# Optimization experiments

Hardware: AMD Instinct MI355X
Metric: run time of the kernel (lower is better)

The kernel has to match this reference:

```python
import jax, jax.numpy as jnp
import numpy as np

B = 32768      # batch
S = 512        # state_dim
G = 128        # goal_dim
A = 32         # action_dim
P = 16         # num_primitives
H1, H2 = 512, 256        # big_model hidden sizes
VH1, VH2 = 1024, 512     # value hidden sizes


def _w(k, shape, scale=0.05):
    return jax.random.normal(k, shape, jnp.float32) * scale


def setup_inputs() -> dict:
    key = jax.random.key(0)
    ks = jax.random.split(key, 24)
    d = {"features": jax.random.normal(ks[0], (B, S + G), jnp.float32)}
    # state encoder: S->H1->H2
    d["se_w1"] = _w(ks[1], (S, H1));  d["se_b1"] = jnp.zeros((H1,), jnp.float32)
    d["se_w2"] = _w(ks[2], (H1, H2)); d["se_b2"] = jnp.zeros((H2,), jnp.float32)
    # goal encoder: G->H1->H2
    d["ge_w1"] = _w(ks[3], (G, H1));  d["ge_b1"] = jnp.zeros((H1,), jnp.float32)
    d["ge_w2"] = _w(ks[4], (H1, H2)); d["ge_b2"] = jnp.zeros((H2,), jnp.float32)
    # gate: 2*H2->H2->P (sigmoid)
    d["gt_w1"] = _w(ks[5], (2 * H2, H2)); d["gt_b1"] = jnp.zeros((H2,), jnp.float32)
    d["gt_w2"] = _w(ks[6], (H2, P));      d["gt_b2"] = jnp.zeros((P,), jnp.float32)
    # primitive state encoder: S->H1->H2
    d["pse_w1"] = _w(ks[7], (S, H1));  d["pse_b1"] = jnp.zeros((H1,), jnp.float32)
    d["pse_w2"] = _w(ks[8], (H1, H2)); d["pse_b2"] = jnp.zeros((H2,), jnp.float32)
    # P primitives, each H2->H2->2A (stacked for batched GEMM)
    d["pw1"] = _w(ks[9], (P, H2, H2));     d["pb1"] = jnp.zeros((P, H2), jnp.float32)
    d["pw2"] = _w(ks[10], (P, H2, 2 * A)); d["pb2"] = jnp.zeros((P, 2 * A), jnp.float32)
    # value net: (S+G)->VH1->VH2
    d["vf_w1"] = _w(ks[11], (S + G, VH1)); d["vf_b1"] = jnp.zeros((VH1,), jnp.float32)
    d["vf_w2"] = _w(ks[12], (VH1, VH2));   d["vf_b2"] = jnp.zeros((VH2,), jnp.float32)
    return d


def _mlp2(x, w1, b1, w2, b2):
    return jax.nn.relu(jax.nn.relu(x @ w1 + b1) @ w2 + b2)


def reference(features,
              se_w1, se_b1, se_w2, se_b2,
              ge_w1, ge_b1, ge_w2, ge_b2,
              gt_w1, gt_b1, gt_w2, gt_b2,
              pse_w1, pse_b1, pse_w2, pse_b2,
              pw1, pb1, pw2, pb2,
              vf_w1, vf_b1, vf_w2, vf_b2):
    state, goal = features[:, :S], features[:, S:]
    # gating weights
    s_emb = _mlp2(state, se_w1, se_b1, se_w2, se_b2)      # [B,H2]
    g_emb = _mlp2(goal, ge_w1, ge_b1, ge_w2, ge_b2)       # [B,H2]
    gate_in = jnp.concatenate([s_emb, g_emb], axis=-1)    # [B,2*H2]
    weights = jax.nn.sigmoid(jax.nn.relu(gate_in @ gt_w1 + gt_b1) @ gt_w2 + gt_b2)  # [B,P]
    # shared primitive embedding
    prim_embed = _mlp2(state, pse_w1, pse_b1, pse_w2, pse_b2)  # [B,H2]
    # all primitives as one batched GEMM
    h = jax.nn.relu(jnp.einsum('bh,phk->bpk', prim_embed, pw1) + pb1[None])  # [B,P,H2]
    out = jnp.einsum('bpk,pkd->bpd', h, pw2) + pb2[None]                      # [B,P,2A]
    mu, log_std = out[..., :A], out[..., A:]
    sigma = jnp.exp(log_std)
    # precision-weighted Gaussian mixture
    inv = weights[..., None] / sigma        # [B,P,A]
    denom = inv.sum(axis=1)                 # [B,A]
    mean = (inv * mu).sum(axis=1) / denom   # [B,A]  (learn_log_std=True -> mean only)
    # critic
    value = _mlp2(features, vf_w1, vf_b1, vf_w2, vf_b2)  # [B,VH2]
    return (mean, value)
```

## Files before the change

kernel.cpp:

```cpp
#include <hip/hip_runtime.h>
#include <stdint.h>

#define NB 32768

typedef __bf16 bf16x8 __attribute__((ext_vector_type(8)));
typedef float f32x4 __attribute__((ext_vector_type(4)));

__device__ __forceinline__ unsigned pack_bf2(float a, float b) {
  union { __bf16 h[2]; unsigned u; } t;
  t.h[0] = (__bf16)a; t.h[1] = (__bf16)b;
  return t.u;
}
__device__ __forceinline__ unsigned short bf16b(float f) {
  union { __bf16 h; unsigned short u; } t;
  t.h = (__bf16)f;
  return t.u;
}
__device__ __forceinline__ float bf2f(unsigned short h) {
  union { unsigned u; float f; } v; v.u = ((unsigned)h) << 16;
  return v.f;
}

__device__ __forceinline__ void gld_lds16(void* lds, const void* g) {
  __builtin_amdgcn_global_load_lds(
      (__attribute__((address_space(1))) unsigned int*)(uintptr_t)g,
      (__attribute__((address_space(3))) unsigned int*)(uintptr_t)lds,
      16, 0, 0);
}

__device__ __forceinline__ int xcd_swz(int bid, int nwg) {
  return (bid & 7) * (nwg >> 3) + (bid >> 3);
}


__global__ __launch_bounds__(256) void fconv_k(const float* __restrict__ src,
                                               unsigned short* __restrict__ dst) {
  size_t idx = ((size_t)blockIdx.x * 256 + threadIdx.x) * 8;
  float4 a = *(const float4*)(src + idx);
  float4 b = *(const float4*)(src + idx + 4);
  uint4 o;
  o.x = pack_bf2(a.x, a.y); o.y = pack_bf2(a.z, a.w);
  o.z = pack_bf2(b.x, b.y); o.w = pack_bf2(b.z, b.w);
  *(uint4*)(dst + idx) = o;
}

__global__ __launch_bounds__(256) void bcat_k(const float* __restrict__ a,
                                              const float* __restrict__ b,
                                              float* __restrict__ dst) {
  const int i = blockIdx.x * 256 + threadIdx.x;
  dst[i] = (i < 512) ? a[i] : b[i - 512];
}

struct TJobs {
  const float* src[11];
  unsigned short* dst[11];
  int K[11], N[11], batch[11];
};

__global__ __launch_bounds__(256) void wtrans_k(TJobs jobs) {
  const int job = blockIdx.y;
  const int K = jobs.K[job], N = jobs.N[job];
  const int KT = K >> 5, NT = N >> 5;
  const int ntiles = jobs.batch[job] * KT * NT;
  const int t = blockIdx.x;
  if (t >= ntiles) return;
  const int b = t / (KT * NT);
  const int rem = t - b * KT * NT;
  const int kt = rem / NT, nt = rem - kt * NT;
  const float* src = jobs.src[job] + (size_t)b * K * N;
  unsigned short* dst = jobs.dst[job] + (size_t)b * K * N;
  __shared__ float tile[32][33];
  const int i = threadIdx.x >> 5, jj = threadIdx.x & 31;
#pragma unroll
  for (int s = 0; s < 4; ++s)
    tile[i + 8 * s][jj] = src[(size_t)(kt * 32 + i + 8 * s) * N + nt * 32 + jj];
  __syncthreads();
#pragma unroll
  for (int s = 0; s < 4; ++s)
    dst[(size_t)(nt * 32 + i + 8 * s) * K + kt * 32 + jj] = bf16b(tile[jj][i + 8 * s]);
}


template <bool OUT_BF16>
__global__ __launch_bounds__(256, 2) void gemm2_k(const unsigned short* __restrict__ A, int lda,
                                                  const unsigned short* __restrict__ WT,
                                                  const float* __restrict__ bias,
                                                  void* __restrict__ Cout, int ldc, int K,
                                                  int ncl2) {
  __shared__ unsigned short a_s[3][128 * 32];
  __shared__ unsigned short b_s[3][256 * 32];
  const int tid = threadIdx.x;
  const int l = tid & 63, w = tid >> 6;
  const int lr = l & 15, lq = l >> 4;
  const int wg = xcd_swz(blockIdx.x, gridDim.x);
  const int col0 = (wg & ((1 << ncl2) - 1)) << 8;
  const int row0 = (wg >> ncl2) << 7;
  const int wbase = tid & ~63;

  auto stage = [&](int t) {
    const int buf = t % 3;
    const int k0 = t << 5;
#pragma unroll
    for (int i = 0; i < 2; ++i) {
      const int s = i * 256 + tid;
      const int r = s >> 2, c = s & 3;
      const int cs = c ^ ((r >> 1) & 3);
      gld_lds16(&a_s[buf][(size_t)(i * 256 + wbase) * 8],
                A + (size_t)(row0 + r) * lda + k0 + cs * 8);
    }
#pragma unroll
    for (int i = 0; i < 4; ++i) {
      const int s = i * 256 + tid;
      const int n = s >> 2, c = s & 3;
      const int cs = c ^ ((n >> 1) & 3);
      gld_lds16(&b_s[buf][(size_t)(i * 256 + wbase) * 8],
                WT + (size_t)(col0 + n) * K + k0 + cs * 8);
    }
  };

  f32x4 acc[8][4] = {};
  const int nt = K >> 5;
  stage(0);
  stage(1);
#pragma unroll 1
  for (int t = 0; t < nt; ++t) {
    if (t + 1 < nt) asm volatile("s_waitcnt vmcnt(6)" ::: "memory");
    else            asm volatile("s_waitcnt vmcnt(0)" ::: "memory");
    __builtin_amdgcn_s_barrier();
    if (t + 2 < nt) stage(t + 2);
    const int cur = t % 3;
    bf16x8 av[8], bv[4];
#pragma unroll
    for (int mf = 0; mf < 8; ++mf) {
      const int r = mf * 16 + lr;
      av[mf] = *(const bf16x8*)&a_s[cur][r * 32 + ((lq ^ ((r >> 1) & 3)) << 3)];
    }
#pragma unroll
    for (int nf = 0; nf < 4; ++nf) {
      const int n = w * 64 + nf * 16 + lr;
      bv[nf] = *(const bf16x8*)&b_s[cur][n * 32 + ((lq ^ ((n >> 1) & 3)) << 3)];
    }
#pragma unroll
    for (int mf = 0; mf < 8; ++mf)
#pragma unroll
      for (int nf = 0; nf < 4; ++nf)
        acc[mf][nf] = __builtin_amdgcn_mfma_f32_16x16x32_bf16(av[mf], bv[nf], acc[mf][nf], 0, 0, 0);
  }

#pragma unroll
  for (int nf = 0; nf < 4; ++nf) {
    const int gc = col0 + w * 64 + nf * 16 + lr;
    const float bb = bias[gc];
#pragma unroll
    for (int mf = 0; mf < 8; ++mf) {
      const int gr = row0 + mf * 16 + (lq << 2);
#pragma unroll
      for (int r = 0; r < 4; ++r) {
        float v = acc[mf][nf][r] + bb;
        v = fmaxf(v, 0.0f);
        if (OUT_BF16)
          ((unsigned short*)Cout)[(size_t)(gr + r) * ldc + gc] = bf16b(v);
        else
          ((float*)Cout)[(size_t)(gr + r) * ldc + gc] = v;
      }
    }
  }
}


template <bool OUT_BF16>
__global__ __launch_bounds__(256, 2) void gemm3_k(const unsigned short* __restrict__ A, int lda,
                                                  const unsigned short* __restrict__ WT,
                                                  const float* __restrict__ bias,
                                                  void* __restrict__ Cout, int ldc, int K,
                                                  int ncl2) {
  __shared__ unsigned short a_s[3][128 * 32];
  __shared__ unsigned short b_s[3][128 * 32];
  const int tid = threadIdx.x;
  const int l = tid & 63, w = tid >> 6;
  const int wm = w >> 1, wn = w & 1;
  const int lr = l & 15, lq = l >> 4;
  const int wg = xcd_swz(blockIdx.x, gridDim.x);
  const int col0 = (wg & ((1 << ncl2) - 1)) << 7;
  const int row0 = (wg >> ncl2) << 7;
  const int wbase = tid & ~63;

  auto stage = [&](int t) {
    const int buf = t % 3;
    const int k0 = t << 5;
#pragma unroll
    for (int i = 0; i < 2; ++i) {
      const int s = i * 256 + tid;
      const int r = s >> 2, c = s & 3;
      const int cs = c ^ ((r >> 1) & 3);
      gld_lds16(&a_s[buf][(size_t)(i * 256 + wbase) * 8],
                A + (size_t)(row0 + r) * lda + k0 + cs * 8);
    }
#pragma unroll
    for (int i = 0; i < 2; ++i) {
      const int s = i * 256 + tid;
      const int n = s >> 2, c = s & 3;
      const int cs = c ^ ((n >> 1) & 3);
      gld_lds16(&b_s[buf][(size_t)(i * 256 + wbase) * 8],
                WT + (size_t)(col0 + n) * K + k0 + cs * 8);
    }
  };

  f32x4 acc[4][4] = {};
  const int nt = K >> 5;
  stage(0);
  stage(1);
#pragma unroll 1
  for (int t = 0; t < nt; ++t) {
    if (t + 1 < nt) asm volatile("s_waitcnt vmcnt(4)" ::: "memory");
    else            asm volatile("s_waitcnt vmcnt(0)" ::: "memory");
    __builtin_amdgcn_s_barrier();
    if (t + 2 < nt) stage(t + 2);
    const int cur = t % 3;
    bf16x8 av[4], bv[4];
#pragma unroll
    for (int mf = 0; mf < 4; ++mf) {
      const int r = wm * 64 + mf * 16 + lr;
      av[mf] = *(const bf16x8*)&a_s[cur][r * 32 + ((lq ^ ((r >> 1) & 3)) << 3)];
    }
#pragma unroll
    for (int nf = 0; nf < 4; ++nf) {
      const int n = wn * 64 + nf * 16 + lr;
      bv[nf] = *(const bf16x8*)&b_s[cur][n * 32 + ((lq ^ ((n >> 1) & 3)) << 3)];
    }
#pragma unroll
    for (int mf = 0; mf < 4; ++mf)
#pragma unroll
      for (int nf = 0; nf < 4; ++nf)
        acc[mf][nf] = __builtin_amdgcn_mfma_f32_16x16x32_bf16(av[mf], bv[nf], acc[mf][nf], 0, 0, 0);
  }

#pragma unroll
  for (int nf = 0; nf < 4; ++nf) {
    const int gc = col0 + wn * 64 + nf * 16 + lr;
    const float bb = bias[gc];
#pragma unroll
    for (int mf = 0; mf < 4; ++mf) {
      const int gr = row0 + wm * 64 + mf * 16 + (lq << 2);
#pragma unroll
      for (int r = 0; r < 4; ++r) {
        float v = acc[mf][nf][r] + bb;
        v = fmaxf(v, 0.0f);
        if (OUT_BF16)
          ((unsigned short*)Cout)[(size_t)(gr + r) * ldc + gc] = bf16b(v);
        else
          ((float*)Cout)[(size_t)(gr + r) * ldc + gc] = v;
      }
    }
  }
}


__global__ __launch_bounds__(256) void gt2_k(const unsigned short* __restrict__ gate_h,
                                             const float* __restrict__ w2,
                                             const float* __restrict__ b2,
                                             float* __restrict__ wgt) {
  __shared__ float w_s[256 * 16];
  __shared__ unsigned short a_s[16 * 264];
  const int tid = threadIdx.x;
  const int row0 = blockIdx.x * 16;
  for (int i = tid; i < 256 * 16; i += 256) w_s[i] = w2[i];
  for (int i = tid; i < 512; i += 256) {
    const int r = i >> 5, cg = i & 31;
    *(uint4*)&a_s[r * 264 + cg * 8] =
        *(const uint4*)(gate_h + (size_t)(row0 + r) * 256 + cg * 8);
  }
  __syncthreads();
  const int rr = tid >> 4, col = tid & 15;
  float sum = b2[col];
#pragma unroll 8
  for (int k = 0; k < 256; ++k)
    sum += bf2f(a_s[rr * 264 + k]) * w_s[k * 16 + col];
  wgt[(size_t)(row0 + rr) * 16 + col] = 1.0f / (1.0f + __expf(-sum));
}


__global__ __launch_bounds__(512, 4) void prim_head_k(
    const unsigned short* __restrict__ prim,
    const float* __restrict__ wgt,
    const unsigned short* __restrict__ pw1t,
    const float* __restrict__ pb1,
    const unsigned short* __restrict__ pw2t,
    const float* __restrict__ pb2,
    float* __restrict__ outbuf)
{
  __shared__ unsigned short prim_s[2][128 * 32];
  __shared__ unsigned short w1_s[2][128 * 32];
  __shared__ unsigned short h_s[128 * 128];
  __shared__ unsigned short pw2_s[64 * 128];
  const int tid = threadIdx.x;
  const int l = tid & 63;
  const int w = tid >> 6;
  const int lr = l & 15, lq = l >> 4;
  const int wn2 = w & 1, wr2 = w >> 1;
  const int row0 = blockIdx.x << 7;
  const int pg = blockIdx.y;
  const int p0 = pg << 3;
  const int wbase = tid & ~63;

  auto stage_ab = [&](const unsigned short* w1p_, int t) {
    const int buf = t & 1;
    const int k0 = (t & 7) << 5;
    const int nb2 = (t >> 3) << 7;
    const int rw = tid >> 2, kc = tid & 3;
    const int kcs = kc ^ ((rw >> 1) & 3);
    gld_lds16(&prim_s[buf][(size_t)wbase * 8],
              prim + (size_t)(row0 + rw) * 256 + k0 + kcs * 8);
    gld_lds16(&w1_s[buf][(size_t)wbase * 8],
              w1p_ + (size_t)(nb2 + rw) * 256 + k0 + kcs * 8);
  };
  auto stage_pw2 = [&](const unsigned short* w2p_, int half) {
    const int nbase = half << 7;
#pragma unroll
    for (int i = 0; i < 2; ++i) {
      const int c = i * 512 + tid;
      const int d = c >> 4, kc = c & 15;
      gld_lds16(&pw2_s[(size_t)(i * 512 + wbase) * 8],
                w2p_ + (size_t)d * 256 + nbase + ((kc ^ (d & 7)) << 3));
    }
  };

  stage_ab(pw1t + (size_t)p0 * 65536, 0);
  stage_pw2(pw2t + (size_t)p0 * 16384, 0);

  f32x4 num[2] = {}, den[2] = {};

#pragma unroll 1
  for (int pi = 0; pi < 8; ++pi) {
    const int p = p0 + pi;
    const unsigned short* w1p = pw1t + (size_t)p * 65536;
    const unsigned short* w2p = pw2t + (size_t)p * 16384;

    f32x4 acc2[2][2] = {};

    for (int half = 0; half < 2; ++half) {
      float4 pb1v[4];
#pragma unroll
      for (int nf = 0; nf < 4; ++nf)
        pb1v[nf] = *(const float4*)(pb1 + p * 256 + (half << 7) + wn2 * 64 + nf * 16 + (lq << 2));

      f32x4 acc1[4][2] = {};
#pragma unroll 1
      for (int ks = 0; ks < 8; ++ks) {
        const int t = (half << 3) + ks;
        const int cur = t & 1;
        asm volatile("s_waitcnt vmcnt(0)" ::: "memory");
        __builtin_amdgcn_s_barrier();
        if (t < 15) stage_ab(w1p, t + 1);
        else if (pi < 7) stage_ab(w1p + 65536, 0);
        bf16x8 av[4], bv[2];
#pragma unroll
        for (int nf = 0; nf < 4; ++nf) {
          const int n = wn2 * 64 + nf * 16 + lr;
          av[nf] = *(const bf16x8*)&w1_s[cur][n * 32 + ((lq ^ ((n >> 1) & 3)) << 3)];
        }
#pragma unroll
        for (int rf = 0; rf < 2; ++rf) {
          const int r = wr2 * 32 + rf * 16 + lr;
          bv[rf] = *(const bf16x8*)&prim_s[cur][r * 32 + ((lq ^ ((r >> 1) & 3)) << 3)];
        }
#pragma unroll
        for (int nf = 0; nf < 4; ++nf)
#pragma unroll
          for (int rf = 0; rf < 2; ++rf)
            acc1[nf][rf] = __builtin_amdgcn_mfma_f32_16x16x32_bf16(av[nf], bv[rf], acc1[nf][rf], 0, 0, 0);
      }

#pragma unroll
      for (int nf = 0; nf < 4; ++nf) {
        const int n0 = wn2 * 64 + nf * 16 + (lq << 2);
        const float4 bb = pb1v[nf];
#pragma unroll
        for (int rf = 0; rf < 2; ++rf) {
          const int row = wr2 * 32 + rf * 16 + lr;
          uint2 pk;
          pk.x = pack_bf2(fmaxf(acc1[nf][rf][0] + bb.x, 0.0f),
                          fmaxf(acc1[nf][rf][1] + bb.y, 0.0f));
          pk.y = pack_bf2(fmaxf(acc1[nf][rf][2] + bb.z, 0.0f),
                          fmaxf(acc1[nf][rf][3] + bb.w, 0.0f));
          *(uint2*)&h_s[row * 128 + (((n0 >> 3) ^ (row & 7)) << 3) + (n0 & 7)] = pk;
        }
      }
      asm volatile("s_waitcnt lgkmcnt(0)" ::: "memory");
      __builtin_amdgcn_s_barrier();

      {
        const int dmu = wn2 * 16;
        const int row_a = wr2 * 32;
#pragma unroll
        for (int kc8 = 0; kc8 < 4; ++kc8) {
          const int slot = ((kc8 << 2) + lq) ^ (lr & 7);
          const bf16x8 amu = *(const bf16x8*)&pw2_s[(dmu + lr) * 128 + (slot << 3)];
          const bf16x8 als = *(const bf16x8*)&pw2_s[(dmu + 32 + lr) * 128 + (slot << 3)];
          const bf16x8 b0 = *(const bf16x8*)&h_s[(row_a + lr) * 128 + (slot << 3)];
          const bf16x8 b1 = *(const bf16x8*)&h_s[(row_a + 16 + lr) * 128 + (slot << 3)];
          acc2[0][0] = __builtin_amdgcn_mfma_f32_16x16x32_bf16(amu, b0, acc2[0][0], 0, 0, 0);
          acc2[0][1] = __builtin_amdgcn_mfma_f32_16x16x32_bf16(als, b0, acc2[0][1], 0, 0, 0);
          acc2[1][0] = __builtin_amdgcn_mfma_f32_16x16x32_bf16(amu, b1, acc2[1][0], 0, 0, 0);
          acc2[1][1] = __builtin_amdgcn_mfma_f32_16x16x32_bf16(als, b1, acc2[1][1], 0, 0, 0);
        }
      }
      asm volatile("s_waitcnt lgkmcnt(0)" ::: "memory");
      __builtin_amdgcn_s_barrier();
      if (half == 0) stage_pw2(w2p, 1);
      else if (pi < 7) stage_pw2(w2p + 16384, 0);
    }

    {
      const int d0 = wn2 * 16 + (lq << 2);
      const int row_a = wr2 * 32;
      const float4 b2mu = *(const float4*)(pb2 + p * 64 + d0);
      const float4 b2ls = *(const float4*)(pb2 + p * 64 + 32 + d0);
      const float wp0 = wgt[(size_t)(row0 + row_a + lr) * 16 + p];
      const float wp1 = wgt[(size_t)(row0 + row_a + 16 + lr) * 16 + p];
#pragma unroll
      for (int s = 0; s < 2; ++s) {
        const float wp = s ? wp1 : wp0;
        const float mu0 = acc2[s][0][0] + b2mu.x, ls0 = acc2[s][1][0] + b2ls.x;
        const float mu1 = acc2[s][0][1] + b2mu.y, ls1 = acc2[s][1][1] + b2ls.y;
        const float mu2 = acc2[s][0][2] + b2mu.z, ls2 = acc2[s][1][2] + b2ls.z;
        const float mu3 = acc2[s][0][3] + b2mu.w, ls3 = acc2[s][1][3] + b2ls.w;
        const float iv0 = wp * __expf(-ls0), iv1 = wp * __expf(-ls1);
        const float iv2 = wp * __expf(-ls2), iv3 = wp * __expf(-ls3);
        num[s][0] += iv0 * mu0; num[s][1] += iv1 * mu1;
        num[s][2] += iv2 * mu2; num[s][3] += iv3 * mu3;
        den[s][0] += iv0; den[s][1] += iv1;
        den[s][2] += iv2; den[s][3] += iv3;
      }
    }
  }

  {
    const int d0 = wn2 * 16 + (lq << 2);
    const int row_a = wr2 * 32;
#pragma unroll
    for (int s = 0; s < 2; ++s) {
      const int row_g = row0 + row_a + s * 16 + lr;
      float* ob = outbuf + ((size_t)row_g * 2 + pg) * 64;
      *(f32x4*)(ob + d0) = num[s];
      *(f32x4*)(ob + 32 + d0) = den[s];
    }
  }
}


__global__ __launch_bounds__(256) void mix_finish_k(const float* __restrict__ buf,
                                                    float* __restrict__ mean_out) {
  const int gid = blockIdx.x * 256 + threadIdx.x;
  const int row = gid >> 3;
  const int a0 = (gid & 7) * 4;
  const float* rp = buf + (size_t)row * 128;
  const f32x4 n0 = *(const f32x4*)(rp + a0);
  const f32x4 d0 = *(const f32x4*)(rp + 32 + a0);
  const f32x4 n1 = *(const f32x4*)(rp + 64 + a0);
  const f32x4 d1 = *(const f32x4*)(rp + 96 + a0);
  f32x4 res;
  res[0] = (n0[0] + n1[0]) / (d0[0] + d1[0]);
  res[1] = (n0[1] + n1[1]) / (d0[1] + d1[1]);
  res[2] = (n0[2] + n1[2]) / (d0[2] + d1[2]);
  res[3] = (n0[3] + n1[3]) / (d0[3] + d1[3]);
  *(f32x4*)(mean_out + (size_t)row * 32 + a0) = res;
}


extern "C" void kernel_launch(void* const* d_in, const int* in_sizes, int n_in,
                              void* d_out, int out_size, void* d_ws, size_t ws_size,
                              hipStream_t stream) {
  const float* features = (const float*)d_in[0];
  const float* se_w1 = (const float*)d_in[1];
  const float* se_b1 = (const float*)d_in[2];
  const float* se_w2 = (const float*)d_in[3];
  const float* se_b2 = (const float*)d_in[4];
  const float* ge_w1 = (const float*)d_in[5];
  const float* ge_b1 = (const float*)d_in[6];
  const float* ge_w2 = (const float*)d_in[7];
  const float* ge_b2 = (const float*)d_in[8];
  const float* gt_w1 = (const float*)d_in[9];
  const float* gt_b1 = (const float*)d_in[10];
  const float* gt_w2 = (const float*)d_in[11];
  const float* gt_b2 = (const float*)d_in[12];
  const float* pse_w1 = (const float*)d_in[13];
  const float* pse_b1 = (const float*)d_in[14];
  const float* pse_w2 = (const float*)d_in[15];
  const float* pse_b2 = (const float*)d_in[16];
  const float* pw1 = (const float*)d_in[17];
  const float* pb1 = (const float*)d_in[18];
  const float* pw2 = (const float*)d_in[19];
  const float* pb2 = (const float*)d_in[20];
  const float* vf_w1 = (const float*)d_in[21];
  const float* vf_b1 = (const float*)d_in[22];
  const float* vf_w2 = (const float*)d_in[23];
  const float* vf_b2 = (const float*)d_in[24];
  (void)in_sizes; (void)n_in; (void)out_size; (void)ws_size;

  char* base = (char*)d_ws;
  size_t off = 0;
  auto alloc = [&](size_t bytes) -> char* {
    char* p = base + off;
    off += (bytes + 255) & ~(size_t)255;
    return p;
  };
  unsigned short* fbf     = (unsigned short*)alloc((size_t)NB * 640 * 2);
  unsigned short* bufA    = (unsigned short*)alloc((size_t)NB * 1024 * 2);
  unsigned short* g1      = (unsigned short*)alloc((size_t)NB * 512 * 2);
  unsigned short* gate_in = (unsigned short*)alloc((size_t)NB * 512 * 2);
  unsigned short* gate_h  = (unsigned short*)alloc((size_t)NB * 256 * 2);
  unsigned short* prim    = (unsigned short*)alloc((size_t)NB * 256 * 2);
  float* wgt              = (float*)alloc((size_t)NB * 16 * 4);
  unsigned short* wcat1t  = (unsigned short*)alloc((size_t)1024 * 512 * 2);
  float* bcat1            = (float*)alloc(1024 * 4);
  unsigned short* se_w2t  = (unsigned short*)alloc(256 * 512 * 2);
  unsigned short* ge_w1t  = (unsigned short*)alloc(512 * 128 * 2);
  unsigned short* ge_w2t  = (unsigned short*)alloc(256 * 512 * 2);
  unsigned short* gt_w1t  = (unsigned short*)alloc(256 * 512 * 2);
  unsigned short* pse_w2t = (unsigned short*)alloc(256 * 512 * 2);
  unsigned short* pw1t    = (unsigned short*)alloc((size_t)16 * 256 * 256 * 2);
  unsigned short* pw2t    = (unsigned short*)alloc((size_t)16 * 64 * 256 * 2);
  unsigned short* vf_w1t  = (unsigned short*)alloc(1024 * 640 * 2);
  unsigned short* vf_w2t  = (unsigned short*)alloc(512 * 1024 * 2);

  unsigned short* se_w1t  = wcat1t;
  unsigned short* pse_w1t = wcat1t + 512 * 512;

  float* outbuf = (float*)bufA;

  float* mean_out = (float*)d_out;
  float* value_out = (float*)d_out + (size_t)NB * 32;

  fconv_k<<<dim3(10240), dim3(256), 0, stream>>>(features, fbf);
  bcat_k<<<dim3(4), dim3(256), 0, stream>>>(se_b1, pse_b1, bcat1);

  TJobs jobs;
  auto setj = [&](int i, const float* s, unsigned short* d, int K, int N, int b) {
    jobs.src[i] = s; jobs.dst[i] = d; jobs.K[i] = K; jobs.N[i] = N; jobs.batch[i] = b;
  };
  setj(0, se_w1, se_w1t, 512, 512, 1);
  setj(1, se_w2, se_w2t, 512, 256, 1);
  setj(2, ge_w1, ge_w1t, 128, 512, 1);
  setj(3, ge_w2, ge_w2t, 512, 256, 1);
  setj(4, gt_w1, gt_w1t, 512, 256, 1);
  setj(5, pse_w1, pse_w1t, 512, 512, 1);
  setj(6, pse_w2, pse_w2t, 512, 256, 1);
  setj(7, pw1, pw1t, 256, 256, 16);
  setj(8, pw2, pw2t, 256, 64, 16);
  setj(9, vf_w1, vf_w1t, 640, 1024, 1);
  setj(10, vf_w2, vf_w2t, 1024, 512, 1);
  wtrans_k<<<dim3(1024, 11), dim3(256), 0, stream>>>(jobs);

  gemm2_k<true><<<dim3(1024), dim3(256), 0, stream>>>(fbf, 640, wcat1t, bcat1, bufA, 1024, 512, 2);
  gemm2_k<true><<<dim3(512), dim3(256), 0, stream>>>(fbf + 512, 640, ge_w1t, ge_b1, g1, 512, 128, 1);
  gemm3_k<true><<<dim3(512), dim3(256), 0, stream>>>(bufA, 1024, se_w2t, se_b2, gate_in, 512, 512, 1);
  gemm3_k<true><<<dim3(512), dim3(256), 0, stream>>>(g1, 512, ge_w2t, ge_b2, gate_in + 256, 512, 512, 1);
  gemm3_k<true><<<dim3(512), dim3(256), 0, stream>>>(gate_in, 512, gt_w1t, gt_b1, gate_h, 256, 512, 1);
  gt2_k<<<dim3(2048), dim3(256), 0, stream>>>(gate_h, gt_w2, gt_b2, wgt);
  gemm3_k<true><<<dim3(512), dim3(256), 0, stream>>>(bufA + 512, 1024, pse_w2t, pse_b2, prim, 256, 512, 1);
  gemm2_k<true><<<dim3(1024), dim3(256), 0, stream>>>(fbf, 640, vf_w1t, vf_b1, bufA, 1024, 640, 2);
  gemm2_k<false><<<dim3(512), dim3(256), 0, stream>>>(bufA, 1024, vf_w2t, vf_b2, value_out, 512, 1024, 1);
  prim_head_k<<<dim3(256, 2), dim3(512), 0, stream>>>(prim, wgt, pw1t, pb1, pw2t, pb2, outbuf);
  mix_finish_k<<<dim3(1024), dim3(256), 0, stream>>>(outbuf, mean_out);
}
```

Measured before the change: 424.7 us.

## Load prim fragments directly to registers and deepen W1 LDS pipeline to four buffers

The primitive-head kernel no longer stages the prim activations through LDS. Each wave loads its MFMA B-operand fragments straight from global memory into double-buffered registers. W1 tiles now use a four-slot LDS ring prefetched two steps ahead, with partial vmcnt waits in place of full drains, and the k-loops are fully unrolled. The goal is to cut LDS traffic and hide global latency better. The cost is more registers, and the kernel issues redundant prefetches for a clamped next primitive on the last iteration.

```diff
diff --git a/kernel.cpp b/kernel.cpp
--- a/kernel.cpp
+++ b/kernel.cpp
@@ -289,8 +289,7 @@
     const float* __restrict__ pb2,
     float* __restrict__ outbuf)
 {
-  __shared__ unsigned short prim_s[2][128 * 32];
-  __shared__ unsigned short w1_s[2][128 * 32];
+  __shared__ unsigned short w1_s[4][128 * 32];
   __shared__ unsigned short h_s[128 * 128];
   __shared__ unsigned short pw2_s[64 * 128];
   const int tid = threadIdx.x;
@@ -303,16 +302,19 @@
   const int p0 = pg << 3;
   const int wbase = tid & ~63;
 
-  auto stage_ab = [&](const unsigned short* w1p_, int t) {
-    const int buf = t & 1;
-    const int k0 = (t & 7) << 5;
-    const int nb2 = (t >> 3) << 7;
-    const int rw = tid >> 2, kc = tid & 3;
-    const int kcs = kc ^ ((rw >> 1) & 3);
-    gld_lds16(&prim_s[buf][(size_t)wbase * 8],
-              prim + (size_t)(row0 + rw) * 256 + k0 + kcs * 8);
-    gld_lds16(&w1_s[buf][(size_t)wbase * 8],
-              w1p_ + (size_t)(nb2 + rw) * 256 + k0 + kcs * 8);
+  const unsigned short* pbase = prim + (size_t)(row0 + wr2 * 32 + lr) * 256 + lq * 8;
+
+  bf16x8 pvA[2], pvB[2];
+  auto ldpv = [&](bf16x8* dst, int kq) {
+#pragma unroll
+    for (int rf = 0; rf < 2; ++rf)
+      dst[rf] = *(const bf16x8*)(pbase + rf * 16 * 256 + kq * 32);
+  };
+  auto stage_w1 = [&](const unsigned short* w1p_, int tt) {
+    const int n = tid >> 2, kc = tid & 3;
+    const int kcs = kc ^ ((n >> 1) & 3);
+    gld_lds16(&w1_s[tt & 3][(size_t)wbase * 8],
+              w1p_ + (size_t)(((tt >> 3) & 1) * 128 + n) * 256 + (tt & 7) * 32 + kcs * 8);
   };
   auto stage_pw2 = [&](const unsigned short* w2p_, int half) {
     const int nbase = half << 7;
@@ -325,7 +327,10 @@
     }
   };
 
-  stage_ab(pw1t + (size_t)p0 * 65536, 0);
+  stage_w1(pw1t + (size_t)p0 * 65536, 0);
+  ldpv(pvA, 0);
+  __builtin_amdgcn_sched_barrier(0);
+  stage_w1(pw1t + (size_t)p0 * 65536, 1);
   stage_pw2(pw2t + (size_t)p0 * 16384, 0);
 
   f32x4 num[2] = {}, den[2] = {};
@@ -333,48 +338,45 @@
 #pragma unroll 1
   for (int pi = 0; pi < 8; ++pi) {
     const int p = p0 + pi;
-    const unsigned short* w1p = pw1t + (size_t)p * 65536;
-    const unsigned short* w2p = pw2t + (size_t)p * 16384;
+    const unsigned short* w1p  = pw1t + (size_t)p * 65536;
+    const unsigned short* w1pn = pw1t + (size_t)(p + 1 < 16 ? p + 1 : 15) * 65536;
+    const unsigned short* w2p  = pw2t + (size_t)p * 16384;
+    const unsigned short* w2pn = pw2t + (size_t)(p + 1 < 16 ? p + 1 : 15) * 16384;
 
     f32x4 acc2[2][2] = {};
 
+#pragma unroll
     for (int half = 0; half < 2; ++half) {
-      float4 pb1v[4];
-#pragma unroll
-      for (int nf = 0; nf < 4; ++nf)
-        pb1v[nf] = *(const float4*)(pb1 + p * 256 + (half << 7) + wn2 * 64 + nf * 16 + (lq << 2));
-
       f32x4 acc1[4][2] = {};
-#pragma unroll 1
+#pragma unroll
       for (int ks = 0; ks < 8; ++ks) {
-        const int t = (half << 3) + ks;
-        const int cur = t & 1;
-        asm volatile("s_waitcnt vmcnt(0)" ::: "memory");
+        const int t = half * 8 + ks;
+        if ((t & 1) == 0) ldpv(pvB, (t + 1) & 7);
+        else              ldpv(pvA, (t + 1) & 7);
+        __builtin_amdgcn_sched_barrier(0);
+        if (t == 0 || t == 8) asm volatile("s_waitcnt vmcnt(5)" ::: "memory");
+        else                  asm volatile("s_waitcnt vmcnt(3)" ::: "memory");
         __builtin_amdgcn_s_barrier();
-        if (t < 15) stage_ab(w1p, t + 1);
-        else if (pi < 7) stage_ab(w1p + 65536, 0);
-        bf16x8 av[4], bv[2];
+        if (t < 14) stage_w1(w1p, t + 2);
+        else        stage_w1(w1pn, t - 14);
+        bf16x8 av[4];
 #pragma unroll
         for (int nf = 0; nf < 4; ++nf) {
           const int n = wn2 * 64 + nf * 16 + lr;
-          av[nf] = *(const bf16x8*)&w1_s[cur][n * 32 + ((lq ^ ((n >> 1) & 3)) << 3)];
+          av[nf] = *(const bf16x8*)&w1_s[t & 3][n * 32 + ((lq ^ ((n >> 1) & 3)) << 3)];
         }
 #pragma unroll
-        for (int rf = 0; rf < 2; ++rf) {
-          const int r = wr2 * 32 + rf * 16 + lr;
-          bv[rf] = *(const bf16x8*)&prim_s[cur][r * 32 + ((lq ^ ((r >> 1) & 3)) << 3)];
-        }
-#pragma unroll
         for (int nf = 0; nf < 4; ++nf)
 #pragma unroll
           for (int rf = 0; rf < 2; ++rf)
-            acc1[nf][rf] = __builtin_amdgcn_mfma_f32_16x16x32_bf16(av[nf], bv[rf], acc1[nf][rf], 0, 0, 0);
+            acc1[nf][rf] = __builtin_amdgcn_mfma_f32_16x16x32_bf16(
+                av[nf], (t & 1) ? pvB[rf] : pvA[rf], acc1[nf][rf], 0, 0, 0);
       }
 
 #pragma unroll
       for (int nf = 0; nf < 4; ++nf) {
         const int n0 = wn2 * 64 + nf * 16 + (lq << 2);
-        const float4 bb = pb1v[nf];
+        const float4 bb = *(const float4*)(pb1 + p * 256 + (half << 7) + n0);
 #pragma unroll
         for (int rf = 0; rf < 2; ++rf) {
           const int row = wr2 * 32 + rf * 16 + lr;
@@ -408,7 +410,7 @@
       asm volatile("s_waitcnt lgkmcnt(0)" ::: "memory");
       __builtin_amdgcn_s_barrier();
       if (half == 0) stage_pw2(w2p, 1);
-      else if (pi < 7) stage_pw2(w2p + 16384, 0);
+      else           stage_pw2(w2pn, 0);
     }
 
     {
```

Result: slower. 527.5 us (+24.2%).

## Use 256x256-tile 512-thread GEMM kernel for the two wide first-layer GEMMs

Applied to the files above, without the earlier changes.

Adds gemm4_k, a bf16 MFMA GEMM with 256x256 output tiles computed by 8 waves (2x4 warp grid), with double-buffered LDS staging via global_load_lds and XOR-swizzled layout. It replaces gemm2_k for the concatenated state/primitive first layer and the value first layer (N=1024), halving the grid. The larger tile raises arithmetic intensity per LDS/global load, at the cost of 64 KB LDS per block and high register pressure from 32 accumulators per thread, which may limit occupancy against the declared launch bounds.

```diff
diff --git a/kernel.cpp b/kernel.cpp
--- a/kernel.cpp
+++ b/kernel.cpp
@@ -154,6 +154,91 @@
 #pragma unroll
     for (int mf = 0; mf < 8; ++mf) {
       const int gr = row0 + mf * 16 + (lq << 2);
+#pragma unroll
+      for (int r = 0; r < 4; ++r) {
+        float v = acc[mf][nf][r] + bb;
+        v = fmaxf(v, 0.0f);
+        if (OUT_BF16)
+          ((unsigned short*)Cout)[(size_t)(gr + r) * ldc + gc] = bf16b(v);
+        else
+          ((float*)Cout)[(size_t)(gr + r) * ldc + gc] = v;
+      }
+    }
+  }
+}
+
+
+template <bool OUT_BF16>
+__global__ __launch_bounds__(512, 4) void gemm4_k(const unsigned short* __restrict__ A, int lda,
+                                                  const unsigned short* __restrict__ WT,
+                                                  const float* __restrict__ bias,
+                                                  void* __restrict__ Cout, int ldc, int K,
+                                                  int ncl2) {
+  __shared__ unsigned short a_s[2][256 * 32];
+  __shared__ unsigned short b_s[2][256 * 32];
+  const int tid = threadIdx.x;
+  const int l = tid & 63, w = tid >> 6;
+  const int wm = w >> 2, wn = w & 3;
+  const int lr = l & 15, lq = l >> 4;
+  const int wg = xcd_swz(blockIdx.x, gridDim.x);
+  const int col0 = (wg & ((1 << ncl2) - 1)) << 8;
+  const int row0 = (wg >> ncl2) << 8;
+  const int wbase = tid & ~63;
+
+  auto stage = [&](int buf, int t) {
+    const int k0 = t << 5;
+#pragma unroll
+    for (int i = 0; i < 2; ++i) {
+      const int s = i * 512 + tid;
+      const int r = s >> 2, c = s & 3;
+      const int cs = c ^ ((r >> 1) & 3);
+      gld_lds16(&a_s[buf][(size_t)(i * 512 + wbase) * 8],
+                A + (size_t)(row0 + r) * lda + k0 + cs * 8);
+    }
+#pragma unroll
+    for (int i = 0; i < 2; ++i) {
+      const int s = i * 512 + tid;
+      const int n = s >> 2, c = s & 3;
+      const int cs = c ^ ((n >> 1) & 3);
+      gld_lds16(&b_s[buf][(size_t)(i * 512 + wbase) * 8],
+                WT + (size_t)(col0 + n) * K + k0 + cs * 8);
+    }
+  };
+
+  f32x4 acc[8][4] = {};
+  const int nt = K >> 5;
+  stage(0, 0);
+  __syncthreads();
+#pragma unroll 1
+  for (int t = 0; t < nt; ++t) {
+    const int cur = t & 1;
+    if (t + 1 < nt) stage(cur ^ 1, t + 1);
+    bf16x8 av[8], bv[4];
+#pragma unroll
+    for (int mf = 0; mf < 8; ++mf) {
+      const int r = wm * 128 + mf * 16 + lr;
+      av[mf] = *(const bf16x8*)&a_s[cur][r * 32 + ((lq ^ ((r >> 1) & 3)) << 3)];
+    }
+#pragma unroll
+    for (int nf = 0; nf < 4; ++nf) {
+      const int n = wn * 64 + nf * 16 + lr;
+      bv[nf] = *(const bf16x8*)&b_s[cur][n * 32 + ((lq ^ ((n >> 1) & 3)) << 3)];
+    }
+#pragma unroll
+    for (int mf = 0; mf < 8; ++mf)
+#pragma unroll
+      for (int nf = 0; nf < 4; ++nf)
+        acc[mf][nf] = __builtin_amdgcn_mfma_f32_16x16x32_bf16(av[mf], bv[nf], acc[mf][nf], 0, 0, 0);
+    __syncthreads();
+  }
+
+#pragma unroll
+  for (int nf = 0; nf < 4; ++nf) {
+    const int gc = col0 + wn * 64 + nf * 16 + lr;
+    const float bb = bias[gc];
+#pragma unroll
+    for (int mf = 0; mf < 8; ++mf) {
+      const int gr = row0 + wm * 128 + mf * 16 + (lq << 2);
 #pragma unroll
       for (int r = 0; r < 4; ++r) {
         float v = acc[mf][nf][r] + bb;
@@ -552,14 +637,14 @@
   setj(10, vf_w2, vf_w2t, 1024, 512, 1);
   wtrans_k<<<dim3(1024, 11), dim3(256), 0, stream>>>(jobs);
 
-  gemm2_k<true><<<dim3(1024), dim3(256), 0, stream>>>(fbf, 640, wcat1t, bcat1, bufA, 1024, 512, 2);
+  gemm4_k<true><<<dim3(512), dim3(512), 0, stream>>>(fbf, 640, wcat1t, bcat1, bufA, 1024, 512, 2);
   gemm2_k<true><<<dim3(512), dim3(256), 0, stream>>>(fbf + 512, 640, ge_w1t, ge_b1, g1, 512, 128, 1);
   gemm3_k<true><<<dim3(512), dim3(256), 0, stream>>>(bufA, 1024, se_w2t, se_b2, gate_in, 512, 512, 1);
   gemm3_k<true><<<dim3(512), dim3(256), 0, stream>>>(g1, 512, ge_w2t, ge_b2, gate_in + 256, 512, 512, 1);
   gemm3_k<true><<<dim3(512), dim3(256), 0, stream>>>(gate_in, 512, gt_w1t, gt_b1, gate_h, 256, 512, 1);
   gt2_k<<<dim3(2048), dim3(256), 0, stream>>>(gate_h, gt_w2, gt_b2, wgt);
   gemm3_k<true><<<dim3(512), dim3(256), 0, stream>>>(bufA + 512, 1024, pse_w2t, pse_b2, prim, 256, 512, 1);
-  gemm2_k<true><<<dim3(1024), dim3(256), 0, stream>>>(fbf, 640, vf_w1t, vf_b1, bufA, 1024, 640, 2);
+  gemm4_k<true><<<dim3(512), dim3(512), 0, stream>>>(fbf, 640, vf_w1t, vf_b1, bufA, 1024, 640, 2);
   gemm2_k<false><<<dim3(512), dim3(256), 0, stream>>>(bufA, 1024, vf_w2t, vf_b2, value_out, 512, 1024, 1);
   prim_head_k<<<dim3(256, 2), dim3(512), 0, stream>>>(prim, wgt, pw1t, pb1, pw2t, pb2, outbuf);
   mix_finish_k<<<dim3(1024), dim3(256), 0, stream>>>(outbuf, mean_out);
```

After: 847.4 us. 99.5% more time.
